# Optimization experiments

Measured on AMD Instinct MI355X. Metric: run time of the kernel, lower is better.

The kernel has to match this reference:

```python
import jax, jax.numpy as jnp
import numpy as np

B, T, N, D, H = 16, 16, 184, 128, 8
HD = D // H  # 16
EMB = 10


def _forward(dim, query, key, value, Wq, bq, Wk, bk, Wv, bv, Wm, bm, Wo, bo, ne1, ne2):
    B0 = query.shape[0]
    D0 = Wq.shape[0]
    HD0 = Wm.shape[0]
    H0 = D0 // HD0
    q = query @ Wq.T + bq
    k = key @ Wk.T + bk
    v = value @ Wv.T + bv

    def split_heads(x):  # [B, A, C, D] -> [H*B, A, C, HD], head-major (torch split+cat)
        x = x.reshape(x.shape[:-1] + (H0, HD0))
        x = jnp.moveaxis(x, -2, 0)  # [H, B, A, C, HD]
        return x.reshape((H0 * B0,) + x.shape[2:])

    q, k, v = split_heads(q), split_heads(k), split_heads(v)
    # attention over the last spatial axis: scores [H*B, T, N, N]
    attn = jnp.matmul(q, jnp.swapaxes(k, -1, -2)) / jnp.sqrt(jnp.asarray(HD0, q.dtype))
    attn_row = jax.nn.softmax(attn, axis=-1)
    attn_col = jax.nn.softmax(attn, axis=-2)
    o1 = jnp.matmul(attn_row, v)
    o2 = jnp.matmul(jnp.swapaxes(attn_col, -1, -2), v)
    adp = ne1 @ ne2  # [184, 184]
    adp_row = jax.nn.softmax(adp, axis=-1)
    adp_col = jax.nn.softmax(adp, axis=0)
    if dim == 2:
        o3 = jnp.einsum('ik,btkf->btif', adp_row, v)
        o4 = jnp.einsum('ik,btkf->btif', adp_col.T, v)
        out = jnp.concatenate([o1, o2, o3, o4], axis=-1)  # [H*B, T, N, 4*HD]
        out = out @ Wm.T + bm  # [H*B, T, N, HD]
    else:  # dim == 1
        o3 = jnp.einsum('ik,bktf->bitf', adp_row, v)
        o4 = jnp.einsum('ik,bktf->bitf', adp_col.T, v)
        cat = jnp.concatenate([o1, o2, o3, o4], axis=-1)
        filt = cat @ Wm.T + bm
        gate = jnp.tanh(cat[..., :HD0]) * jax.nn.sigmoid(cat[..., -HD0:])
        out = filt + gate
    # merge heads back: [H*B, ..., HD] -> [B, ..., H*HD]
    out = out.reshape((H0, B0) + out.shape[1:])
    out = jnp.moveaxis(out, 0, -2)
    out = out.reshape(out.shape[:-2] + (H0 * HD0,))
    return out @ Wo.T + bo


def setup_inputs() -> dict:
    rng = jax.random.key(0)
    ks = jax.random.split(rng, 16)
    n = lambda i, shape, s=1.0: jax.random.normal(ks[i], shape, dtype=jnp.float32) * s
    return {
        'query': n(0, (B, T, N, D)),
        'key': n(1, (B, T, N, D)),
        'value': n(2, (B, T, N, D)),
        'Wq': n(3, (D, D), 0.05), 'bq': n(4, (D,), 0.05),
        'Wk': n(5, (D, D), 0.05), 'bk': n(6, (D,), 0.05),
        'Wv': n(7, (D, D), 0.05), 'bv': n(8, (D,), 0.05),
        'Wm': n(9, (HD, 4 * HD), 0.05), 'bm': n(10, (HD,), 0.05),
        'Wo': n(11, (D, D), 0.05), 'bo': n(12, (D,), 0.05),
        'ne1': n(13, (N, EMB)),
        'ne2': n(14, (EMB, N)),
        'dim': 2,
    }


def reference(query, key, value, Wq, bq, Wk, bk, Wv, bv, Wm, bm, Wo, bo, ne1, ne2, dim):
    return _forward(dim, query, key, value, Wq, bq, Wk, bk, Wv, bv, Wm, bm, Wo, bo, ne1, ne2)
```

## Files before the change

kernel.cpp:

```cpp
#include <hip/hip_runtime.h>

typedef unsigned int u32;
typedef unsigned short u16;
typedef unsigned long long ull;

constexpr int kB = 16, kT = 16, kN = 184, kD = 128, kH = 8, kHD = 16;
constexpr int kBT = kB * kT;
constexpr int kRows = kBT * kN;
constexpr int kTile = kN * kHD;
#define KQSCALE 0.36067376022224085f

typedef __attribute__((ext_vector_type(8))) short bf16x8;
typedef __attribute__((ext_vector_type(4))) float f32x4;

union FragU {
  bf16x8 f;
  ull u[2];
  uint4 q;
  u16 h[8];
};

#define MFMA(a, b, c) __builtin_amdgcn_mfma_f32_16x16x32_bf16((a), (b), (c), 0, 0, 0)

__device__ __forceinline__ float bf2f(u16 v) {
  return __uint_as_float(((u32)v) << 16);
}
__device__ __forceinline__ u16 f2bf(float f) {
  u32 x = __float_as_uint(f);
  x += 0x7fffu + ((x >> 16) & 1u);
  return (u16)(x >> 16);
}
__device__ __forceinline__ u32 pack_bf2(float lo, float hi) {
  u32 a = __float_as_uint(lo); a += 0x7fffu + ((a >> 16) & 1u);
  u32 b = __float_as_uint(hi); b += 0x7fffu + ((b >> 16) & 1u);
  return __builtin_amdgcn_perm(b, a, 0x07060302);
}
__device__ __forceinline__ u32 pack_trunc(float lo, float hi) {
  return __builtin_amdgcn_perm(__float_as_uint(hi), __float_as_uint(lo), 0x07060302);
}
__device__ __forceinline__ u16 trunc_bf(float f) {
  return (u16)(__float_as_uint(f) >> 16);
}

__global__ __launch_bounds__(256) void wcvt_kernel(
    const float* __restrict__ Wq, const float* __restrict__ Wk,
    const float* __restrict__ Wv, const float* __restrict__ Wo,
    u16* __restrict__ wb) {
  const int t = blockIdx.x * 256 + threadIdx.x;
  if (t >= 8192) return;
  u32* dst = (u32*)wb;
  float2 a = ((const float2*)Wq)[t]; dst[t]          = pack_bf2(a.x, a.y);
  float2 b = ((const float2*)Wk)[t]; dst[8192 + t]   = pack_bf2(b.x, b.y);
  float2 c = ((const float2*)Wv)[t]; dst[16384 + t]  = pack_bf2(c.x, c.y);
  float2 d = ((const float2*)Wo)[t]; dst[24576 + t]  = pack_bf2(d.x, d.y);
}

__global__ __launch_bounds__(256) void adp_kernel(
    const float* __restrict__ ne1, const float* __restrict__ ne2,
    u16* __restrict__ arr3, u16* __restrict__ arr4) {
  __shared__ float s1[kN * 10];
  __shared__ float s2[10 * kN];
  __shared__ float l1r[kN];
  __shared__ float l2c[kN];
  const int tid = threadIdx.x;
  for (int i = tid; i < kN * 10; i += 256) { s1[i] = ne1[i]; s2[i] = ne2[i]; }
  __syncthreads();

  if (tid < kN) {
    const int r = tid;
    float reg[10];
#pragma unroll
    for (int e = 0; e < 10; ++e) reg[e] = s1[r * 10 + e];
    float sum = 0.f;
    for (int c = 0; c < kN; ++c) {
      float d = 0.f;
#pragma unroll
      for (int e = 0; e < 10; ++e) d += reg[e] * s2[e * kN + c];
      sum += __expf(d);
    }
    l1r[r] = sum;

    const int c = tid;
    float regc[10];
#pragma unroll
    for (int e = 0; e < 10; ++e) regc[e] = s2[e * kN + c];
    sum = 0.f;
    for (int r2 = 0; r2 < kN; ++r2) {
      float d = 0.f;
#pragma unroll
      for (int e = 0; e < 10; ++e) d += s1[r2 * 10 + e] * regc[e];
      sum += __expf(d);
    }
    l2c[c] = sum;
  }
  __syncthreads();

  for (int ee = blockIdx.x * 256 + tid; ee < 12 * 6 * 64; ee += 12 * 256) {
    const int i = ee / 384;
    const int rem = ee - i * 384;
    const int p = rem >> 6;
    const int lane = rem & 63;
    const int row = i * 16 + (lane & 15);
    const int cb = p * 32 + (lane >> 4) * 8;
    FragU fo3, fo4;
    const bool rok = row < kN;
    float inv1 = 0.f, inv2 = 0.f;
    float rreg[10], creg[10];
    if (rok) {
      inv1 = 1.f / l1r[row];
      inv2 = 1.f / l2c[row];
#pragma unroll
      for (int e = 0; e < 10; ++e) {
        rreg[e] = s1[row * 10 + e];
        creg[e] = s2[e * kN + row];
      }
    }
#pragma unroll
    for (int j = 0; j < 8; ++j) {
      const int col = cb + j;
      float v3 = 0.f, v4 = 0.f;
      if (rok && col < kN) {
        float d3 = 0.f, d4 = 0.f;
#pragma unroll
        for (int e = 0; e < 10; ++e) {
          d3 += rreg[e] * s2[e * kN + col];
          d4 += s1[col * 10 + e] * creg[e];
        }
        v3 = __expf(d3) * inv1;
        v4 = __expf(d4) * inv2;
      }
      fo3.h[j] = f2bf(v3);
      fo4.h[j] = f2bf(v4);
    }
    *(uint4*)(arr3 + (size_t)ee * 8) = fo3.q;
    *(uint4*)(arr4 + (size_t)ee * 8) = fo4.q;
  }
}

__global__ __launch_bounds__(256) void proj_kernel(
    const float* __restrict__ qin, const float* __restrict__ kin, const float* __restrict__ vin,
    const u16* __restrict__ wb,
    const float* __restrict__ bq, const float* __restrict__ bk, const float* __restrict__ bv,
    u16* __restrict__ qo, u16* __restrict__ ko, u16* __restrict__ vo) {
  __shared__ u16 s_w[128 * 136];

  const float* in; const u16* W; const float* bias; u16* out; float scale;
  if (blockIdx.y == 0)      { in = qin; W = wb;         bias = bq; out = qo; scale = KQSCALE; }
  else if (blockIdx.y == 1) { in = kin; W = wb + 16384; bias = bk; out = ko; scale = 1.f; }
  else                      { in = vin; W = wb + 32768; bias = bv; out = vo; scale = 1.f; }

  const int tid = threadIdx.x;
  {
    const uint4* src = (const uint4*)W;
    for (int i = tid; i < 2048; i += 256) {
      const int row = i >> 4, q16 = i & 15;
      *(uint4*)(s_w + row * 136 + q16 * 8) = src[i];
    }
  }
  __syncthreads();

  const int w = tid >> 6, lane = tid & 63, quad = lane >> 4, m = lane & 15;
  const int r0 = blockIdx.x * 128;

  f32x4 acc0[8], acc1[8];
  const f32x4 z4 = {0.f, 0.f, 0.f, 0.f};
#pragma unroll
  for (int ct = 0; ct < 8; ++ct) { acc0[ct] = z4; acc1[ct] = z4; }

  const float* xp0 = in + (size_t)(r0 + w * 16 + m) * 128 + quad * 8;
  const float* xp1 = xp0 + 64 * 128;

#pragma unroll
  for (int kp = 0; kp < 4; ++kp) {
    const float4 xa = *(const float4*)(xp0 + kp * 32);
    const float4 xb = *(const float4*)(xp0 + kp * 32 + 4);
    const float4 ya = *(const float4*)(xp1 + kp * 32);
    const float4 yb = *(const float4*)(xp1 + kp * 32 + 4);
    FragU a0, a1;
    a0.q = make_uint4(pack_bf2(xa.x, xa.y), pack_bf2(xa.z, xa.w),
                      pack_bf2(xb.x, xb.y), pack_bf2(xb.z, xb.w));
    a1.q = make_uint4(pack_bf2(ya.x, ya.y), pack_bf2(ya.z, ya.w),
                      pack_bf2(yb.x, yb.y), pack_bf2(yb.z, yb.w));
#pragma unroll
    for (int ct = 0; ct < 8; ++ct) {
      FragU bfr; bfr.q = *(const uint4*)(s_w + (ct * 16 + m) * 136 + kp * 32 + quad * 8);
      acc0[ct] = MFMA(a0.f, bfr.f, acc0[ct]);
      acc1[ct] = MFMA(a1.f, bfr.f, acc1[ct]);
    }
  }

  float bc[8];
#pragma unroll
  for (int ct = 0; ct < 8; ++ct) bc[ct] = bias[ct * 16 + m];

#pragma unroll
  for (int half = 0; half < 2; ++half) {
    const f32x4* acc = half ? acc1 : acc0;
    const int rbase = r0 + (w + half * 4) * 16 + quad * 4;
#pragma unroll
    for (int rr = 0; rr < 4; ++rr) {
      const int r = rbase + rr;
      const int bt = r / kN;
      const int n = r - bt * kN;
      u16* op = out + ((size_t)bt * kN + n) * 16 + m;
#pragma unroll
      for (int ct = 0; ct < 8; ++ct)
        op[(size_t)ct * kBT * kN * 16] = f2bf((acc[ct][rr] + bc[ct]) * scale);
    }
  }
}

__global__ __launch_bounds__(256, 2) void attn_kernel(
    const u16* qg, const u16* __restrict__ kg, const u16* __restrict__ vg,
    const u16* __restrict__ arr3, const u16* __restrict__ arr4,
    const float* __restrict__ Wm, const float* __restrict__ bm,
    u16* mg) {
  __shared__ u16 s_vT[16 * 200];
  __shared__ u16 s_E[192 * 72];
  __shared__ u16 s_ET[64 * 200];
  __shared__ u16 s_cat[4 * 1152];

  const int tid = threadIdx.x;
  const size_t base = (size_t)blockIdx.x * kTile;
  const int w = tid >> 6, lane = tid & 63;
  const int quad = lane >> 4, m = lane & 15;

  for (int idx = tid; idx < 3072; idx += 256) {
    const int t = idx >> 4, ch = idx & 15;
    s_vT[ch * 200 + t] = (t < kN) ? vg[base + idx] : (u16)0;
  }

  bf16x8 kfr[12];
#pragma unroll
  for (int t12 = 0; t12 < 12; ++t12) {
    FragU fk; fk.u[0] = 0; fk.u[1] = 0;
    const int tok = t12 * 16 + m;
    if (quad < 2 && tok < kN)
      fk.q = *(const uint4*)(kg + base + tok * 16 + quad * 8);
    kfr[t12] = fk.f;
  }
  bf16x8 qB[3];
#pragma unroll
  for (int ti = 0; ti < 3; ++ti) {
    FragU fq; fq.u[0] = 0; fq.u[1] = 0;
    const int tok = (w + ti * 4) * 16 + m;
    if (quad < 2 && tok < kN)
      fq.q = *(const uint4*)(qg + base + tok * 16 + quad * 8);
    qB[ti] = fq.f;
  }

  bf16x8 wmb[2];
#pragma unroll
  for (int kt = 0; kt < 2; ++kt) {
    FragU f;
#pragma unroll
    for (int j = 0; j < 8; ++j) {
      const int kdl = quad * 8 + j;
      const int orig = (kt * 2 + (kdl & 1)) * 16 + (kdl >> 1);
      f.h[j] = f2bf(Wm[m * 64 + orig]);
    }
    wmb[kt] = f.f;
  }
  const float4 bm4 = *(const float4*)(bm + quad * 4);

  __syncthreads();

  bf16x8 vb[6];
#pragma unroll
  for (int p = 0; p < 6; ++p) {
    FragU f;
    f.q = *(const uint4*)(s_vT + m * 200 + p * 32 + quad * 8);
    vb[p] = f.f;
  }
  FragU onesU; onesU.u[0] = 0x3F803F803F803F80ULL; onesU.u[1] = onesU.u[0];
  const bf16x8 ones = onesU.f;
  const f32x4 zero4 = {0.f, 0.f, 0.f, 0.f};

  f32x4 o1[3], l1[3], o3[3], o4[3], o2[3], l2[3];
#pragma unroll
  for (int ti = 0; ti < 3; ++ti) {
    o1[ti] = zero4; l1[ti] = zero4; o3[ti] = zero4;
    o4[ti] = zero4; o2[ti] = zero4; l2[ti] = zero4;
  }

#define S_PHASE(CC)                                                           \
  do {                                                                        \
    _Pragma("unroll") for (int ti = 0; ti < 3; ++ti) {                        \
      const int qt = w + ti * 4;                                              \
      const int qrow = qt * 16 + m;                                           \
      _Pragma("unroll") for (int ktl = 0; ktl < 4; ++ktl) {                   \
        f32x4 sv = MFMA(kfr[(CC) * 4 + ktl], qB[ti], zero4);                  \
        const float e0 = exp2f(sv[0]), e1 = exp2f(sv[1]);                     \
        const float e2 = exp2f(sv[2]), e3 = exp2f(sv[3]);                     \
        uint2 ev;                                                             \
        ev.x = pack_trunc(e0, e1);                                            \
        ev.y = pack_trunc(e2, e3);                                            \
        *(uint2*)(s_E + qrow * 72 + ktl * 16 + quad * 4) = ev;                \
        u16* etp = s_ET + (ktl * 16 + quad * 4) * 200 + qrow;                 \
        etp[0]   = trunc_bf(e0);                                              \
        etp[200] = trunc_bf(e1);                                              \
        etp[400] = trunc_bf(e2);                                              \
        etp[600] = trunc_bf(e3);                                              \
      }                                                                       \
    }                                                                         \
  } while (0)

#define R_PHASE(CC)                                                           \
  do {                                                                        \
    _Pragma("unroll") for (int ti = 0; ti < 3; ++ti) {                        \
      const int qt = w + ti * 4;                                              \
      const u16* erp = s_E + (qt * 16 + m) * 72 + quad * 8;                   \
      _Pragma("unroll") for (int pl = 0; pl < 2; ++pl) {                      \
        const int pg = (CC) * 2 + pl;                                         \
        FragU pa; pa.q = *(const uint4*)(erp + pl * 32);                      \
        o1[ti] = MFMA(pa.f, vb[pg], o1[ti]);                                  \
        l1[ti] = MFMA(pa.f, ones, l1[ti]);                                    \
        FragU a3; a3.q = *(const uint4*)(arr3 + (size_t)((qt * 6 + pg) * 64 + lane) * 8); \
        FragU a4; a4.q = *(const uint4*)(arr4 + (size_t)((qt * 6 + pg) * 64 + lane) * 8); \
        o3[ti] = MFMA(a3.f, vb[pg], o3[ti]);                                  \
        o4[ti] = MFMA(a4.f, vb[pg], o4[ti]);                                  \
      }                                                                       \
    }                                                                         \
    {                                                                         \
      const u16* etr = s_ET + (w * 16 + m) * 200 + quad * 8;                  \
      _Pragma("unroll") for (int pg = 0; pg < 6; ++pg) {                      \
        FragU pT; pT.q = *(const uint4*)(etr + pg * 32);                      \
        o2[CC] = MFMA(pT.f, vb[pg], o2[CC]);                                  \
        l2[CC] = MFMA(pT.f, ones, l2[CC]);                                    \
      }                                                                       \
    }                                                                         \
  } while (0)

  S_PHASE(0);
  __syncthreads();
  R_PHASE(0);
  __syncthreads();
  S_PHASE(1);
  __syncthreads();
  R_PHASE(1);
  __syncthreads();
  S_PHASE(2);
  __syncthreads();
  R_PHASE(2);

#undef S_PHASE
#undef R_PHASE

  u16* cw = s_cat + w * 1152;
#pragma unroll
  for (int ti = 0; ti < 3; ++ti) {
    const int tt = w + ti * 4;
#pragma unroll
    for (int r = 0; r < 4; ++r) {
      const int token = quad * 4 + r;
      const float n1 = o1[ti][r] * __builtin_amdgcn_rcpf(l1[ti][r] - 8.0f);
      const float n2 = o2[ti][r] * __builtin_amdgcn_rcpf(l2[ti][r] - 8.0f);
      *(u32*)(cw + token * 72 + 2 * m)      = pack_bf2(n1, n2);
      *(u32*)(cw + token * 72 + 32 + 2 * m) = pack_bf2(o3[ti][r], o4[ti][r]);
    }
    f32x4 macc = {bm4.x, bm4.y, bm4.z, bm4.w};
#pragma unroll
    for (int kt = 0; kt < 2; ++kt) {
      FragU ca; ca.q = *(const uint4*)(cw + m * 72 + kt * 32 + quad * 8);
      macc = MFMA(wmb[kt], ca.f, macc);
    }
    if (tt * 16 + m < kN) {
      *(uint2*)(mg + base + (tt * 16 + m) * 16 + quad * 4) =
          make_uint2(pack_bf2(macc[0], macc[1]), pack_bf2(macc[2], macc[3]));
    }
  }
}

__global__ __launch_bounds__(256) void out_kernel(
    const u16* __restrict__ mg, const u16* __restrict__ wob,
    const float* __restrict__ bo, float* __restrict__ outg) {
  __shared__ u16 s_w[128 * 136];
  const int tid = threadIdx.x;
  {
    const uint4* src = (const uint4*)wob;
    for (int i = tid; i < 2048; i += 256) {
      const int row = i >> 4, q16 = i & 15;
      *(uint4*)(s_w + row * 136 + q16 * 8) = src[i];
    }
  }
  __syncthreads();

  const int w = tid >> 6, lane = tid & 63, quad = lane >> 4, m = lane & 15;
  const int r0 = blockIdx.x * 128;

  f32x4 acc0[8], acc1[8];
  const f32x4 z4 = {0.f, 0.f, 0.f, 0.f};
#pragma unroll
  for (int ct = 0; ct < 8; ++ct) { acc0[ct] = z4; acc1[ct] = z4; }

  const int hh = quad >> 1, hd8 = (quad & 1) * 8;
  const int ra = r0 + w * 16 + m;
  const int bt0 = ra / kN, n0 = ra - bt0 * kN;
  const int rb = ra + 64;
  const int bt1 = rb / kN, n1 = rb - bt1 * kN;
  const u16* mp0 = mg + ((size_t)(hh * kBT + bt0) * kN + n0) * 16 + hd8;
  const u16* mp1 = mg + ((size_t)(hh * kBT + bt1) * kN + n1) * 16 + hd8;
  const size_t hstep = (size_t)2 * kBT * kN * 16;

#pragma unroll
  for (int kp = 0; kp < 4; ++kp) {
    FragU a0; a0.q = *(const uint4*)(mp0 + kp * hstep);
    FragU a1; a1.q = *(const uint4*)(mp1 + kp * hstep);
#pragma unroll
    for (int ct = 0; ct < 8; ++ct) {
      FragU bfr; bfr.q = *(const uint4*)(s_w + (ct * 16 + m) * 136 + kp * 32 + quad * 8);
      acc0[ct] = MFMA(a0.f, bfr.f, acc0[ct]);
      acc1[ct] = MFMA(a1.f, bfr.f, acc1[ct]);
    }
  }

  float bc[8];
#pragma unroll
  for (int ct = 0; ct < 8; ++ct) bc[ct] = bo[ct * 16 + m];

#pragma unroll
  for (int half = 0; half < 2; ++half) {
    const f32x4* acc = half ? acc1 : acc0;
    const int rbase = r0 + (w + half * 4) * 16 + quad * 4;
#pragma unroll
    for (int rr = 0; rr < 4; ++rr) {
      float* op = outg + (size_t)(rbase + rr) * 128 + m;
#pragma unroll
      for (int ct = 0; ct < 8; ++ct)
        op[ct * 16] = acc[ct][rr] + bc[ct];
    }
  }
}

extern "C" void kernel_launch(void* const* d_in, const int* in_sizes, int n_in,
                              void* d_out, int out_size, void* d_ws, size_t ws_size,
                              hipStream_t stream) {
  const float* query = (const float*)d_in[0];
  const float* key   = (const float*)d_in[1];
  const float* value = (const float*)d_in[2];
  const float* Wq = (const float*)d_in[3];
  const float* bq = (const float*)d_in[4];
  const float* Wk = (const float*)d_in[5];
  const float* bk = (const float*)d_in[6];
  const float* Wv = (const float*)d_in[7];
  const float* bv = (const float*)d_in[8];
  const float* Wm = (const float*)d_in[9];
  const float* bm = (const float*)d_in[10];
  const float* Wo = (const float*)d_in[11];
  const float* bo = (const float*)d_in[12];
  const float* ne1 = (const float*)d_in[13];
  const float* ne2 = (const float*)d_in[14];

  const size_t tensor_bytes = (size_t)kH * kB * kT * kN * kHD * 2;
  const size_t frag_bytes = (size_t)12 * 6 * 64 * 8 * 2;
  char* ws = (char*)d_ws;
  u16* qs   = (u16*)(ws);
  u16* ks   = (u16*)(ws + tensor_bytes);
  u16* vs   = (u16*)(ws + 2 * tensor_bytes);
  u16* arr3 = (u16*)(ws + 3 * tensor_bytes);
  u16* arr4 = (u16*)(ws + 3 * tensor_bytes + frag_bytes);
  u16* wb   = (u16*)(ws + 3 * tensor_bytes + 2 * frag_bytes);

  wcvt_kernel<<<32, 256, 0, stream>>>(Wq, Wk, Wv, Wo, wb);
  adp_kernel<<<12, 256, 0, stream>>>(ne1, ne2, arr3, arr4);
  proj_kernel<<<dim3(kRows / 128, 3), 256, 0, stream>>>(
      query, key, value, wb, bq, bk, bv, qs, ks, vs);
  attn_kernel<<<kH * kB * kT, 256, 0, stream>>>(qs, ks, vs, arr3, arr4, Wm, bm, qs);
  out_kernel<<<kRows / 128, 256, 0, stream>>>(qs, wb + 49152, bo, (float*)d_out);
}
```

Baseline: 242.5 us.

## Double-buffer transposed score tile and overlap next score phase with reductions

The separate shared arrays are folded into one pool. The transposed exponent buffer is now double-buffered, and the V-transpose and concat scratch areas alias the second buffer. Each chunk's column and row MFMA reductions now run in the same barrier interval as the next chunk's score/exp phase, with the arr3/arr4 global fragment loads issued up front. This cuts the per-block barrier count and shared memory footprint, aiming to overlap exp and LDS writes with MFMA work. The cost is more live registers, since the fragment arrays are held across the phase.

Result: no change. 240.5 us (-0.8%).

```diff
diff --git a/kernel.cpp b/kernel.cpp
--- a/kernel.cpp
+++ b/kernel.cpp
@@ -215,10 +215,12 @@
     const u16* __restrict__ arr3, const u16* __restrict__ arr4,
     const float* __restrict__ Wm, const float* __restrict__ bm,
     u16* mg) {
-  __shared__ u16 s_vT[16 * 200];
-  __shared__ u16 s_E[192 * 72];
-  __shared__ u16 s_ET[64 * 200];
-  __shared__ u16 s_cat[4 * 1152];
+  __shared__ u16 pool[39424];
+  u16* const s_E   = pool;
+  u16* const s_ET0 = pool + 13824;
+  u16* const s_ET1 = pool + 26624;
+  u16* const s_vT  = s_ET1;
+  u16* const s_cat = s_ET1;
 
   const int tid = threadIdx.x;
   const size_t base = (size_t)blockIdx.x * kTile;
@@ -283,7 +285,7 @@
     o4[ti] = zero4; o2[ti] = zero4; l2[ti] = zero4;
   }
 
-#define S_PHASE(CC)                                                           \
+#define S_PHASE(CC, ETB)                                                      \
   do {                                                                        \
     _Pragma("unroll") for (int ti = 0; ti < 3; ++ti) {                        \
       const int qt = w + ti * 4;                                              \
@@ -296,7 +298,7 @@
         ev.x = pack_trunc(e0, e1);                                            \
         ev.y = pack_trunc(e2, e3);                                            \
         *(uint2*)(s_E + qrow * 72 + ktl * 16 + quad * 4) = ev;                \
-        u16* etp = s_ET + (ktl * 16 + quad * 4) * 200 + qrow;                 \
+        u16* etp = (ETB) + (ktl * 16 + quad * 4) * 200 + qrow;                \
         etp[0]   = trunc_bf(e0);                                              \
         etp[200] = trunc_bf(e1);                                              \
         etp[400] = trunc_bf(e2);                                              \
@@ -305,46 +307,69 @@
     }                                                                         \
   } while (0)
 
-#define R_PHASE(CC)                                                           \
-  do {                                                                        \
-    _Pragma("unroll") for (int ti = 0; ti < 3; ++ti) {                        \
-      const int qt = w + ti * 4;                                              \
-      const u16* erp = s_E + (qt * 16 + m) * 72 + quad * 8;                   \
-      _Pragma("unroll") for (int pl = 0; pl < 2; ++pl) {                      \
-        const int pg = (CC) * 2 + pl;                                         \
-        FragU pa; pa.q = *(const uint4*)(erp + pl * 32);                      \
-        o1[ti] = MFMA(pa.f, vb[pg], o1[ti]);                                  \
-        l1[ti] = MFMA(pa.f, ones, l1[ti]);                                    \
-        FragU a3; a3.q = *(const uint4*)(arr3 + (size_t)((qt * 6 + pg) * 64 + lane) * 8); \
-        FragU a4; a4.q = *(const uint4*)(arr4 + (size_t)((qt * 6 + pg) * 64 + lane) * 8); \
-        o3[ti] = MFMA(a3.f, vb[pg], o3[ti]);                                  \
-        o4[ti] = MFMA(a4.f, vb[pg], o4[ti]);                                  \
-      }                                                                       \
+#define LOAD_ARR(CC)                                                          \
+  _Pragma("unroll") for (int ti = 0; ti < 3; ++ti) {                          \
+    const int qt = w + ti * 4;                                                \
+    _Pragma("unroll") for (int pl = 0; pl < 2; ++pl) {                        \
+      const int pg = (CC) * 2 + pl;                                           \
+      a3f[ti * 2 + pl].q = *(const uint4*)(arr3 + (size_t)((qt * 6 + pg) * 64 + lane) * 8); \
+      a4f[ti * 2 + pl].q = *(const uint4*)(arr4 + (size_t)((qt * 6 + pg) * 64 + lane) * 8); \
     }                                                                         \
-    {                                                                         \
-      const u16* etr = s_ET + (w * 16 + m) * 200 + quad * 8;                  \
-      _Pragma("unroll") for (int pg = 0; pg < 6; ++pg) {                      \
-        FragU pT; pT.q = *(const uint4*)(etr + pg * 32);                      \
-        o2[CC] = MFMA(pT.f, vb[pg], o2[CC]);                                  \
-        l2[CC] = MFMA(pT.f, ones, l2[CC]);                                    \
-      }                                                                       \
+  }
+
+#define ROW_PHASE(CC)                                                         \
+  _Pragma("unroll") for (int ti = 0; ti < 3; ++ti) {                          \
+    const int qt = w + ti * 4;                                                \
+    const u16* erp = s_E + (qt * 16 + m) * 72 + quad * 8;                     \
+    _Pragma("unroll") for (int pl = 0; pl < 2; ++pl) {                        \
+      const int pg = (CC) * 2 + pl;                                           \
+      FragU pa; pa.q = *(const uint4*)(erp + pl * 32);                        \
+      o1[ti] = MFMA(pa.f, vb[pg], o1[ti]);                                    \
+      l1[ti] = MFMA(pa.f, ones, l1[ti]);                                      \
+      o3[ti] = MFMA(a3f[ti * 2 + pl].f, vb[pg], o3[ti]);                      \
+      o4[ti] = MFMA(a4f[ti * 2 + pl].f, vb[pg], o4[ti]);                      \
     }                                                                         \
-  } while (0)
-
-  S_PHASE(0);
-  __syncthreads();
-  R_PHASE(0);
-  __syncthreads();
-  S_PHASE(1);
-  __syncthreads();
-  R_PHASE(1);
-  __syncthreads();
-  S_PHASE(2);
-  __syncthreads();
-  R_PHASE(2);
+  }
+
+#define COL_PHASE(CC, ETB)                                                    \
+  {                                                                           \
+    const u16* etr = (ETB) + (w * 16 + m) * 200 + quad * 8;                   \
+    _Pragma("unroll") for (int pg = 0; pg < 6; ++pg) {                        \
+      FragU pT; pT.q = *(const uint4*)(etr + pg * 32);                        \
+      o2[CC] = MFMA(pT.f, vb[pg], o2[CC]);                                    \
+      l2[CC] = MFMA(pT.f, ones, l2[CC]);                                      \
+    }                                                                         \
+  }
+
+  S_PHASE(0, s_ET0);
+  __syncthreads();
+  {
+    FragU a3f[6], a4f[6];
+    LOAD_ARR(0);
+    COL_PHASE(0, s_ET0);
+    ROW_PHASE(0);
+    S_PHASE(1, s_ET1);
+  }
+  __syncthreads();
+  {
+    FragU a3f[6], a4f[6];
+    LOAD_ARR(1);
+    COL_PHASE(1, s_ET1);
+    ROW_PHASE(1);
+    S_PHASE(2, s_ET0);
+  }
+  __syncthreads();
+  {
+    FragU a3f[6], a4f[6];
+    LOAD_ARR(2);
+    COL_PHASE(2, s_ET0);
+    ROW_PHASE(2);
+  }
 
 #undef S_PHASE
-#undef R_PHASE
+#undef LOAD_ARR
+#undef ROW_PHASE
+#undef COL_PHASE
 
   u16* cw = s_cat + w * 1152;
 #pragma unroll
```
